# Kernel tuning notes

Measured on AMD Instinct MI355X. Metric: run time of the kernel, lower is better.

Reference implementation:

```python
import jax, jax.numpy as jnp
import numpy as np

NUM_USER = 10000
NUM_ITEM = 30000
N = NUM_USER + NUM_ITEM          # total nodes
DIM = 64                          # dim_E == dim_C
E = 500000                        # user-item interactions
NUM_ROUTING = 3
ALPHA_THR = 0.5
NEG_SLOPE_ATTN = 0.2              # GAT attention leaky slope
NEG_SLOPE_ACT = 0.01              # F.leaky_relu_ default


def l2norm(x, eps=1e-12):
    n = jnp.linalg.norm(x, axis=-1, keepdims=True)
    return x / jnp.maximum(n, eps)


def seg_softmax(score, seg):
    # numerically-stable softmax over edges grouped by destination node
    m = jax.ops.segment_max(score, seg, num_segments=N)
    e = jnp.exp(score - m[seg])
    s = jax.ops.segment_sum(e, seg, num_segments=N)
    return e / (s[seg] + 1e-16)


def gat_ori(x, W, src, dst):
    # GATConv_ori: dot-product attention, softmax per destination, scatter-add
    h = x @ W                                     # [N, C]
    score = jax.nn.leaky_relu(jnp.sum(h[dst] * h[src], -1), NEG_SLOPE_ATTN)
    alpha = seg_softmax(score, dst)               # [2E]
    return jax.ops.segment_sum(alpha[:, None] * h[src], dst, num_segments=N)


def gat_pre(x, y, z, W, src, dst):
    # GATConv_pre: primary-modality attention modulated by cross-modal gate (reattn)
    hx = x @ W
    sx = jnp.sum(hx[dst] * hx[src], -1)
    sy = jnp.sum(y[dst] * y[src], -1)
    sz = jnp.sum(z[dst] * z[src], -1)
    alpha = seg_softmax(jax.nn.leaky_relu(sx, NEG_SLOPE_ATTN), dst)
    gate = jax.nn.sigmoid(0.5 * (sy + sz))
    alpha = jnp.where(gate > ALPHA_THR, alpha * gate, alpha)
    return jax.ops.segment_sum(alpha[:, None] * hx[src], dst, num_segments=N)


def cgcn(pref, feat, pref2, feat2, pref3, feat3, src, dst, Wpre, Wori):
    x = jnp.concatenate([pref, feat], 0)
    y = jnp.concatenate([pref2, feat2], 0)
    z = jnp.concatenate([pref3, feat3], 0)
    x = l2norm(gat_pre(x, y, z, Wpre, src, dst))
    for _ in range(NUM_ROUTING):
        x = l2norm(x + gat_ori(x, Wori, src, dst))
    return x


def gcn_conv(x, W, src, dst):
    return jax.ops.segment_sum((x @ W)[src], dst, num_segments=N)


def real_gcn(id_emb, Wg, src, dst):
    x = l2norm(id_emb)
    h1 = jax.nn.leaky_relu(gcn_conv(x, Wg[0], src, dst), NEG_SLOPE_ACT)
    h2 = jax.nn.leaky_relu(gcn_conv(h1, Wg[1], src, dst), NEG_SLOPE_ACT)
    h3 = gcn_conv(h1, Wg[2], src, dst)
    return x + h1 + h2 + h3


def setup_inputs() -> dict:
    key = jax.random.key(0)
    ks = jax.random.split(key, 16)
    users = jax.random.randint(ks[0], (E,), 0, NUM_USER)
    items = jax.random.randint(ks[1], (E,), NUM_USER, N)
    edge_index = jnp.stack([users, items]).astype(jnp.int64)
    s = 0.05
    return {
        'edge_index': edge_index,
        'v_feat': jax.random.normal(ks[2], (NUM_ITEM, 128), jnp.float32),
        'a_feat': jax.random.normal(ks[3], (NUM_ITEM, 128), jnp.float32),
        't_feat': jax.random.normal(ks[4], (NUM_ITEM, 100), jnp.float32),
        'pref_v': jax.random.normal(ks[5], (NUM_USER, DIM), jnp.float32) * s,
        'pref_a': jax.random.normal(ks[6], (NUM_USER, DIM), jnp.float32) * s,
        'pref_t': jax.random.normal(ks[7], (NUM_USER, DIM), jnp.float32) * s,
        'mlp_v_w': jax.random.normal(ks[8], (DIM, 128), jnp.float32) * s,
        'mlp_v_b': jnp.zeros((DIM,), jnp.float32),
        'mlp_a_w': jax.random.normal(ks[9], (DIM, 128), jnp.float32) * s,
        'mlp_a_b': jnp.zeros((DIM,), jnp.float32),
        'mlp_t_w': jax.random.normal(ks[10], (DIM, 100), jnp.float32) * s,
        'mlp_t_b': jnp.zeros((DIM,), jnp.float32),
        'pre_w': jax.random.normal(ks[11], (3, DIM, DIM), jnp.float32) * s,
        'ori_w': jax.random.normal(ks[12], (3, DIM, DIM), jnp.float32) * s,
        'gcn_w': jax.random.normal(ks[13], (3, DIM, DIM), jnp.float32) * s,
        'id_embedding': jax.random.normal(ks[14], (N, DIM), jnp.float32) * s,
    }


def reference(edge_index, v_feat, a_feat, t_feat, pref_v, pref_a, pref_t,
              mlp_v_w, mlp_v_b, mlp_a_w, mlp_a_b, mlp_t_w, mlp_t_b,
              pre_w, ori_w, gcn_w, id_embedding):
    # symmetrize edges (cat with flipped); no self-loops possible (bipartite)
    src = jnp.concatenate([edge_index[0], edge_index[1]])
    dst = jnp.concatenate([edge_index[1], edge_index[0]])

    fv = l2norm(jax.nn.leaky_relu(v_feat @ mlp_v_w.T + mlp_v_b, NEG_SLOPE_ACT))
    fa = l2norm(jax.nn.leaky_relu(a_feat @ mlp_a_w.T + mlp_a_b, NEG_SLOPE_ACT))
    ft = l2norm(jax.nn.leaky_relu(t_feat @ mlp_t_w.T + mlp_t_b, NEG_SLOPE_ACT))
    pv, pa, pt = l2norm(pref_v), l2norm(pref_a), l2norm(pref_t)

    v_rep = cgcn(pv, fv, pa, fa, pt, ft, src, dst, pre_w[0], ori_w[0])
    a_rep = cgcn(pa, fa, pv, fv, pt, ft, src, dst, pre_w[1], ori_w[1])
    t_rep = cgcn(pt, ft, pa, fa, pv, fv, src, dst, pre_w[2], ori_w[2])
    id_rep = real_gcn(id_embedding, gcn_w, src, dst)

    return jnp.concatenate([id_rep, v_rep, a_rep, t_rep], axis=1)  # [N, 4*DIM]
```

## Files before the change

kernel.cpp:

```cpp
#include <hip/hip_runtime.h>
#include <hip/hip_fp16.h>
#include <math.h>

#define NUSER 10000
#define NITEM 30000
#define NN    40000
#define DD    64
#define PLANE ((size_t)NN * DD)

typedef _Float16 hv2 __attribute__((ext_vector_type(2)));
union U2H { unsigned u; hv2 v; __half2 hh; };

#if defined(__has_builtin)
#if __has_builtin(__builtin_amdgcn_fdot2)
#define HAS_FDOT2 1
#endif
#endif

__device__ __forceinline__ float fdot2u(unsigned a, unsigned b, float c) {
#ifdef HAS_FDOT2
    U2H x, y;
    x.u = a;
    y.u = b;
    return __builtin_amdgcn_fdot2(x.v, y.v, c, false);
#else
    U2H x, y;
    x.u = a;
    y.u = b;
    float2 fa = __half22float2(x.hh), fb = __half22float2(y.hh);
    return c + fa.x * fb.x + fa.y * fb.y;
#endif
}

__device__ __forceinline__ float dot8(uint4 a, uint4 b) {
    float d = fdot2u(a.x, b.x, 0.f);
    d = fdot2u(a.y, b.y, d);
    d = fdot2u(a.z, b.z, d);
    d = fdot2u(a.w, b.w, d);
    return d;
}

__device__ __forceinline__ __half2 uh(unsigned u) { U2H x; x.u = u; return x.hh; }
__device__ __forceinline__ unsigned hu(__half2 h) { U2H x; x.hh = h; return x.u; }
__device__ __forceinline__ __half2 h2rx(__half2 v, int m) {
    return __hadd2(v, uh((unsigned)__shfl_xor((int)hu(v), m, 64)));
}

__device__ __forceinline__ float wsum(float v) {
#pragma unroll
    for (int o = 32; o > 0; o >>= 1) v += __shfl_xor(v, o, 64);
    return v;
}
__device__ __forceinline__ float qsum8(float v) {
    v += __shfl_xor(v, 1, 64);
    v += __shfl_xor(v, 2, 64);
    v += __shfl_xor(v, 4, 64);
    return v;
}
__device__ __forceinline__ float gsum8(float v) {
    v += __shfl_xor(v, 8, 64);
    v += __shfl_xor(v, 16, 64);
    v += __shfl_xor(v, 32, 64);
    return v;
}

__device__ __forceinline__ int nodeperm(int i) {
    return ((i & 3) == 0) ? (i >> 2) : (NUSER + i - 1 - (i >> 2));
}

__global__ void k_hist(const int* ei, int E2, int E, int* cnt) {
    int i = blockIdx.x * blockDim.x + threadIdx.x;
    if (i >= E2) return;
    int d = (i < E) ? ei[E + i] : ei[i - E];
    atomicAdd(&cnt[d], 1);
}

__global__ void k_bsum(const int* __restrict__ cnt, int* __restrict__ bsum, int n, int chunk) {
    __shared__ int wsh[4];
    int b = blockIdx.x, tid = threadIdx.x;
    int base = b * chunk, end = min(n, base + chunk);
    int s = 0;
    for (int i = base + tid; i < end; i += 256) s += cnt[i];
#pragma unroll
    for (int o = 32; o > 0; o >>= 1) s += __shfl_xor(s, o, 64);
    if ((tid & 63) == 0) wsh[tid >> 6] = s;
    __syncthreads();
    if (tid == 0) bsum[b] = wsh[0] + wsh[1] + wsh[2] + wsh[3];
}

__global__ void k_bscan(int* bsum, int nb, int* rp_end) {
    int lane = threadIdx.x;
    int v = (lane < nb) ? bsum[lane] : 0;
    int orig = v;
#pragma unroll
    for (int o = 1; o < 64; o <<= 1) {
        int y = __shfl_up(v, o, 64);
        if (lane >= o) v += y;
    }
    if (lane < nb) bsum[lane] = v - orig;
    if (lane == 63) *rp_end = v;
}

__global__ void k_apply(const int* __restrict__ cnt, const int* __restrict__ boff,
                        int* __restrict__ rp, int n, int chunk) {
    __shared__ int buf[256];
    __shared__ int csh;
    int b = blockIdx.x, tid = threadIdx.x;
    int base = b * chunk, end = min(n, base + chunk);
    int carry = boff[b];
    for (int t0 = base; t0 < end; t0 += 256) {
        int i = t0 + tid;
        int v = (i < end) ? cnt[i] : 0;
        int x = v;
        buf[tid] = x;
        __syncthreads();
        for (int o = 1; o < 256; o <<= 1) {
            int y = (tid >= o) ? buf[tid - o] : 0;
            __syncthreads();
            x += y;
            buf[tid] = x;
            __syncthreads();
        }
        if (i < end) rp[i] = carry + x - v;
        __syncthreads();
        if (tid == 255) csh = carry + x;
        __syncthreads();
        carry = csh;
    }
}

__global__ void k_scatter(const int* ei, int E2, int E, const int* rp, int* fill, int* col) {
    int i = blockIdx.x * blockDim.x + threadIdx.x;
    if (i >= E2) return;
    int j = (i < E) ? i : i - E;
    int s = (i < E) ? ei[j] : ei[E + j];
    int d = (i < E) ? ei[E + j] : ei[j];
    int pos = rp[d] + atomicAdd(&fill[d], 1);
    col[pos] = s;
}

__global__ void k_prep_pref(const float* __restrict__ pv, const float* __restrict__ pa,
                            const float* __restrict__ pt, __half* __restrict__ M) {
    int t = blockIdx.x * blockDim.x + threadIdx.x;
    int w = t >> 6, lane = t & 63, nw = (gridDim.x * blockDim.x) >> 6;
    for (int r = w; r < NUSER; r += nw) {
        float a = pv[(size_t)r * DD + lane];
        float b = pa[(size_t)r * DD + lane];
        float c = pt[(size_t)r * DD + lane];
        float sa = a * a, sb = b * b, sc = c * c;
#pragma unroll
        for (int o = 32; o > 0; o >>= 1) {
            sa += __shfl_xor(sa, o, 64);
            sb += __shfl_xor(sb, o, 64);
            sc += __shfl_xor(sc, o, 64);
        }
        size_t base = (size_t)r * 3 * DD + lane;
        M[base] = __float2half(a / fmaxf(sqrtf(sa), 1e-12f));
        M[base + DD] = __float2half(b / fmaxf(sqrtf(sb), 1e-12f));
        M[base + 2 * DD] = __float2half(c / fmaxf(sqrtf(sc), 1e-12f));
    }
}

template <int K>
__global__ void k_mlp(const float* __restrict__ feat, const float* __restrict__ W,
                      const float* __restrict__ bias, __half* __restrict__ M, int mo) {
    constexpr int K4 = K / 4;
    __shared__ float4 Wl[K4][DD];
    __shared__ float4 rbuf[4][2][K4];
    int t = threadIdx.x, wib = t >> 6, lane = t & 63;
    for (int i = t; i < DD * K4; i += 256) {
        int c = i / K4, k4 = i - c * K4;
        Wl[k4][c] = *(const float4*)(W + (size_t)c * K + k4 * 4);
    }
    __syncthreads();
    float b = bias[lane];
    const int stride = gridDim.x * 4;
    int r = blockIdx.x * 4 + wib;
    float4 v = {0.f, 0.f, 0.f, 0.f};
    if (r < NITEM && lane < K4) v = *(const float4*)(feat + (size_t)r * K + lane * 4);
    int cur = 0;
    for (; r < NITEM; r += stride) {
        if (lane < K4) rbuf[wib][cur][lane] = v;
        int rn = r + stride;
        if (rn < NITEM && lane < K4) v = *(const float4*)(feat + (size_t)rn * K + lane * 4);
        asm volatile("s_waitcnt lgkmcnt(0)" ::: "memory");
        float acc = b;
#pragma unroll
        for (int k4 = 0; k4 < K4; k4++) {
            float4 x4 = rbuf[wib][cur][k4];
            float4 w4 = Wl[k4][lane];
            acc += x4.x * w4.x + x4.y * w4.y + x4.z * w4.z + x4.w * w4.w;
        }
        float h = acc > 0.f ? acc : 0.01f * acc;
        float n = sqrtf(wsum(h * h));
        M[((size_t)(NUSER + r) * 3 + mo) * DD + lane] = __float2half(h / fmaxf(n, 1e-12f));
        cur ^= 1;
    }
}

__global__ void k_gemm_h3(const __half* __restrict__ x3, const float* __restrict__ W3,
                          __half* __restrict__ o3) {
    __shared__ float rowbuf[4][DD];
    int mo = blockIdx.y;
    const float* W = W3 + (size_t)mo * 4096;
    int t = threadIdx.x, wib = t >> 6, lane = t & 63;
    float Wc[DD];
#pragma unroll
    for (int k = 0; k < DD; k++) Wc[k] = W[k * DD + lane];
    for (int r = blockIdx.x * 4 + wib; r < NN; r += gridDim.x * 4) {
        size_t idx = ((size_t)r * 3 + mo) * DD + lane;
        rowbuf[wib][lane] = __half2float(x3[idx]);
        asm volatile("s_waitcnt lgkmcnt(0)" ::: "memory");
        float acc = 0.f;
#pragma unroll
        for (int k4 = 0; k4 < DD / 4; k4++) {
            float4 xq = *(const float4*)&rowbuf[wib][k4 * 4];
            acc += xq.x * Wc[k4 * 4] + xq.y * Wc[k4 * 4 + 1] + xq.z * Wc[k4 * 4 + 2] +
                   xq.w * Wc[k4 * 4 + 3];
        }
        o3[idx] = __float2half(acc);
    }
}

__global__ void k_gemm_f2(const float* __restrict__ x, const float* __restrict__ W2,
                          __half* __restrict__ o2) {
    __shared__ float rowbuf[4][DD];
    int mo = blockIdx.y;
    const float* W = W2 + (size_t)mo * 4096;
    int t = threadIdx.x, wib = t >> 6, lane = t & 63;
    float Wc[DD];
#pragma unroll
    for (int k = 0; k < DD; k++) Wc[k] = W[k * DD + lane];
    for (int r = blockIdx.x * 4 + wib; r < NN; r += gridDim.x * 4) {
        rowbuf[wib][lane] = x[(size_t)r * DD + lane];
        asm volatile("s_waitcnt lgkmcnt(0)" ::: "memory");
        float acc = 0.f;
#pragma unroll
        for (int k4 = 0; k4 < DD / 4; k4++) {
            float4 xq = *(const float4*)&rowbuf[wib][k4 * 4];
            acc += xq.x * Wc[k4 * 4] + xq.y * Wc[k4 * 4 + 1] + xq.z * Wc[k4 * 4 + 2] +
                   xq.w * Wc[k4 * 4 + 3];
        }
        o2[((size_t)r * 2 + mo) * DD + lane] = __float2half(acc);
    }
}

__global__ void k_gemm_id(const float* __restrict__ x, const float* __restrict__ W,
                          __half* __restrict__ hout, float* __restrict__ xnorm) {
    __shared__ float rowbuf[4][DD];
    int t = threadIdx.x, wib = t >> 6, lane = t & 63;
    float Wc[DD];
#pragma unroll
    for (int k = 0; k < DD; k++) Wc[k] = W[k * DD + lane];
    for (int r = blockIdx.x * 4 + wib; r < NN; r += gridDim.x * 4) {
        float xv = x[(size_t)r * DD + lane];
        float n = sqrtf(wsum(xv * xv));
        xv /= fmaxf(n, 1e-12f);
        xnorm[(size_t)r * DD + lane] = xv;
        rowbuf[wib][lane] = xv;
        asm volatile("s_waitcnt lgkmcnt(0)" ::: "memory");
        float acc = 0.f;
#pragma unroll
        for (int k4 = 0; k4 < DD / 4; k4++) {
            float4 xq = *(const float4*)&rowbuf[wib][k4 * 4];
            acc += xq.x * Wc[k4 * 4] + xq.y * Wc[k4 * 4 + 1] + xq.z * Wc[k4 * 4 + 2] +
                   xq.w * Wc[k4 * 4 + 3];
        }
        hout[(size_t)r * DD + lane] = __float2half(acc);
    }
}

__device__ __forceinline__ float gatef(float ssum) {
    float gate = 1.f / (1.f + __expf(-0.5f * ssum));
    return gate > 0.5f ? gate : 1.f;
}

__global__ void k_edgedot3(const __half* __restrict__ M, const int* __restrict__ rp,
                           const int* __restrict__ col, __half* __restrict__ gf4) {
    int t = blockIdx.x * blockDim.x + threadIdx.x;
    int wv = t >> 6, lane = t & 63, nw = (gridDim.x * blockDim.x) >> 6;
    int g = lane >> 3, q = lane & 7;
    for (int w0 = wv; w0 < NN; w0 += nw) {
        int n = nodeperm(w0);
        int e0 = rp[n], e1 = rp[n + 1];
        if (e0 == e1) continue;
        const uint4* trow = (const uint4*)(M + (size_t)n * 192);
        uint4 tv = trow[q], ta = trow[q + 8], tt = trow[q + 16];
        for (int eb = e0 + g; eb < e1; eb += 8) {
            int sn = col[eb];
            const uint4* srow = (const uint4*)(M + (size_t)sn * 192);
            uint4 sv = srow[q], sa = srow[q + 8], st = srow[q + 16];
            float dv = dot8(tv, sv), da = dot8(ta, sa), dt = dot8(tt, st);
            dv = qsum8(dv);
            da = qsum8(da);
            dt = qsum8(dt);
            if (q == 0) {
                U2H p01, p2;
                p01.hh = __floats2half2_rn(gatef(da + dt), gatef(dv + dt));
                p2.hh = __floats2half2_rn(gatef(da + dv), 0.f);
                *(uint2*)(gf4 + (size_t)eb * 4) = make_uint2(p01.u, p2.u);
            }
        }
    }
}

__global__ void k_gat_pre3(const __half* __restrict__ h3, const __half* __restrict__ gf4,
                           const int* __restrict__ rp, const int* __restrict__ col,
                           __half* __restrict__ x3h) {
    int t = blockIdx.x * blockDim.x + threadIdx.x;
    int wv = t >> 6, lane = t & 63, nw = (gridDim.x * blockDim.x) >> 6;
    int g = lane >> 3, q = lane & 7;
    const __half2 z = __floats2half2_rn(0.f, 0.f);
    for (int w0 = wv; w0 < NN; w0 += nw) {
        int n = nodeperm(w0);
        int e0 = rp[n], e1 = rp[n + 1];
        const uint4* hrow = (const uint4*)(h3 + (size_t)n * 192);
        uint4 hd0 = hrow[q], hd1 = hrow[q + 8], hd2 = hrow[q + 16];
        float s0 = 0.f, s1 = 0.f, s2 = 0.f;
        __half2 a0[4] = {z, z, z, z}, a1[4] = {z, z, z, z}, a2[4] = {z, z, z, z};
        for (int eb = e0 + g; eb < e1; eb += 8) {
            int sn = col[eb];
            const uint4* srow = (const uint4*)(h3 + (size_t)sn * 192);
            uint4 v0 = srow[q], v1 = srow[q + 8], v2 = srow[q + 16];
            uint2 gv = *(const uint2*)(gf4 + (size_t)eb * 4);
            float d0 = dot8(hd0, v0), d1 = dot8(hd1, v1), d2 = dot8(hd2, v2);
            d0 = qsum8(d0);
            d1 = qsum8(d1);
            d2 = qsum8(d2);
            float2 g01 = __half22float2(uh(gv.x));
            float g2 = __half22float2(uh(gv.y)).x;
            float sc0 = d0 > 0.f ? d0 : 0.2f * d0;
            float sc1 = d1 > 0.f ? d1 : 0.2f * d1;
            float sc2 = d2 > 0.f ? d2 : 0.2f * d2;
            float p0 = __expf(sc0), p1 = __expf(sc1), p2 = __expf(sc2);
            s0 += p0;
            s1 += p1;
            s2 += p2;
            __half2 ph0 = __float2half2_rn(p0 * g01.x);
            __half2 ph1 = __float2half2_rn(p1 * g01.y);
            __half2 ph2 = __float2half2_rn(p2 * g2);
            a0[0] = __hfma2(ph0, uh(v0.x), a0[0]);
            a0[1] = __hfma2(ph0, uh(v0.y), a0[1]);
            a0[2] = __hfma2(ph0, uh(v0.z), a0[2]);
            a0[3] = __hfma2(ph0, uh(v0.w), a0[3]);
            a1[0] = __hfma2(ph1, uh(v1.x), a1[0]);
            a1[1] = __hfma2(ph1, uh(v1.y), a1[1]);
            a1[2] = __hfma2(ph1, uh(v1.z), a1[2]);
            a1[3] = __hfma2(ph1, uh(v1.w), a1[3]);
            a2[0] = __hfma2(ph2, uh(v2.x), a2[0]);
            a2[1] = __hfma2(ph2, uh(v2.y), a2[1]);
            a2[2] = __hfma2(ph2, uh(v2.z), a2[2]);
            a2[3] = __hfma2(ph2, uh(v2.w), a2[3]);
        }
        s0 = gsum8(s0);
        s1 = gsum8(s1);
        s2 = gsum8(s2);
#pragma unroll
        for (int j = 0; j < 4; j++) {
            a0[j] = h2rx(h2rx(h2rx(a0[j], 8), 16), 32);
            a1[j] = h2rx(h2rx(h2rx(a1[j], 8), 16), 32);
            a2[j] = h2rx(h2rx(h2rx(a2[j], 8), 16), 32);
        }
        float i0 = 1.f / (s0 + 1e-16f), i1 = 1.f / (s1 + 1e-16f), i2 = 1.f / (s2 + 1e-16f);
        float o0[8], o1[8], o2[8];
#pragma unroll
        for (int j = 0; j < 4; j++) {
            float2 f0 = __half22float2(a0[j]);
            float2 f1 = __half22float2(a1[j]);
            float2 f2 = __half22float2(a2[j]);
            o0[2 * j] = f0.x * i0;
            o0[2 * j + 1] = f0.y * i0;
            o1[2 * j] = f1.x * i1;
            o1[2 * j + 1] = f1.y * i1;
            o2[2 * j] = f2.x * i2;
            o2[2 * j + 1] = f2.y * i2;
        }
        float n0 = 0.f, n1 = 0.f, n2 = 0.f;
#pragma unroll
        for (int k = 0; k < 8; k++) {
            n0 += o0[k] * o0[k];
            n1 += o1[k] * o1[k];
            n2 += o2[k] * o2[k];
        }
        n0 = qsum8(n0);
        n1 = qsum8(n1);
        n2 = qsum8(n2);
        float r0 = 1.f / fmaxf(sqrtf(n0), 1e-12f);
        float r1 = 1.f / fmaxf(sqrtf(n1), 1e-12f);
        float r2 = 1.f / fmaxf(sqrtf(n2), 1e-12f);
        if (g == 0) {
            uint4* orow = (uint4*)(x3h + (size_t)n * 192);
            uint4 w0_, w1_, w2_;
            w0_.x = hu(__floats2half2_rn(o0[0] * r0, o0[1] * r0));
            w0_.y = hu(__floats2half2_rn(o0[2] * r0, o0[3] * r0));
            w0_.z = hu(__floats2half2_rn(o0[4] * r0, o0[5] * r0));
            w0_.w = hu(__floats2half2_rn(o0[6] * r0, o0[7] * r0));
            w1_.x = hu(__floats2half2_rn(o1[0] * r1, o1[1] * r1));
            w1_.y = hu(__floats2half2_rn(o1[2] * r1, o1[3] * r1));
            w1_.z = hu(__floats2half2_rn(o1[4] * r1, o1[5] * r1));
            w1_.w = hu(__floats2half2_rn(o1[6] * r1, o1[7] * r1));
            w2_.x = hu(__floats2half2_rn(o2[0] * r2, o2[1] * r2));
            w2_.y = hu(__floats2half2_rn(o2[2] * r2, o2[3] * r2));
            w2_.z = hu(__floats2half2_rn(o2[4] * r2, o2[5] * r2));
            w2_.w = hu(__floats2half2_rn(o2[6] * r2, o2[7] * r2));
            orow[q] = w0_;
            orow[q + 8] = w1_;
            orow[q + 16] = w2_;
        }
    }
}

__global__ void k_gat_ori3(const __half* __restrict__ h3, const __half* __restrict__ x3h,
                           const int* __restrict__ rp, const int* __restrict__ col,
                           __half* __restrict__ xout, float* __restrict__ fout) {
    int t = blockIdx.x * blockDim.x + threadIdx.x;
    int wv = t >> 6, lane = t & 63, nw = (gridDim.x * blockDim.x) >> 6;
    int g = lane >> 3, q = lane & 7;
    const __half2 z = __floats2half2_rn(0.f, 0.f);
    for (int w0 = wv; w0 < NN; w0 += nw) {
        int n = nodeperm(w0);
        int e0 = rp[n], e1 = rp[n + 1];
        const uint4* hrow = (const uint4*)(h3 + (size_t)n * 192);
        uint4 hd0 = hrow[q], hd1 = hrow[q + 8], hd2 = hrow[q + 16];
        float s0 = 0.f, s1 = 0.f, s2 = 0.f;
        __half2 a0[4] = {z, z, z, z}, a1[4] = {z, z, z, z}, a2[4] = {z, z, z, z};
        for (int eb = e0 + g; eb < e1; eb += 8) {
            int sn = col[eb];
            const uint4* srow = (const uint4*)(h3 + (size_t)sn * 192);
            uint4 v0 = srow[q], v1 = srow[q + 8], v2 = srow[q + 16];
            float d0 = dot8(hd0, v0), d1 = dot8(hd1, v1), d2 = dot8(hd2, v2);
            d0 = qsum8(d0);
            d1 = qsum8(d1);
            d2 = qsum8(d2);
            float sc0 = d0 > 0.f ? d0 : 0.2f * d0;
            float sc1 = d1 > 0.f ? d1 : 0.2f * d1;
            float sc2 = d2 > 0.f ? d2 : 0.2f * d2;
            float p0 = __expf(sc0), p1 = __expf(sc1), p2 = __expf(sc2);
            s0 += p0;
            s1 += p1;
            s2 += p2;
            __half2 ph0 = __float2half2_rn(p0);
            __half2 ph1 = __float2half2_rn(p1);
            __half2 ph2 = __float2half2_rn(p2);
            a0[0] = __hfma2(ph0, uh(v0.x), a0[0]);
            a0[1] = __hfma2(ph0, uh(v0.y), a0[1]);
            a0[2] = __hfma2(ph0, uh(v0.z), a0[2]);
            a0[3] = __hfma2(ph0, uh(v0.w), a0[3]);
            a1[0] = __hfma2(ph1, uh(v1.x), a1[0]);
            a1[1] = __hfma2(ph1, uh(v1.y), a1[1]);
            a1[2] = __hfma2(ph1, uh(v1.z), a1[2]);
            a1[3] = __hfma2(ph1, uh(v1.w), a1[3]);
            a2[0] = __hfma2(ph2, uh(v2.x), a2[0]);
            a2[1] = __hfma2(ph2, uh(v2.y), a2[1]);
            a2[2] = __hfma2(ph2, uh(v2.z), a2[2]);
            a2[3] = __hfma2(ph2, uh(v2.w), a2[3]);
        }
        s0 = gsum8(s0);
        s1 = gsum8(s1);
        s2 = gsum8(s2);
#pragma unroll
        for (int j = 0; j < 4; j++) {
            a0[j] = h2rx(h2rx(h2rx(a0[j], 8), 16), 32);
            a1[j] = h2rx(h2rx(h2rx(a1[j], 8), 16), 32);
            a2[j] = h2rx(h2rx(h2rx(a2[j], 8), 16), 32);
        }
        float i0 = 1.f / (s0 + 1e-16f), i1 = 1.f / (s1 + 1e-16f), i2 = 1.f / (s2 + 1e-16f);
        const uint4* xrow = (const uint4*)(x3h + (size_t)n * 192);
        uint4 xr0 = xrow[q], xr1 = xrow[q + 8], xr2 = xrow[q + 16];
        float o0[8], o1[8], o2[8];
#pragma unroll
        for (int j = 0; j < 4; j++) {
            float2 f0 = __half22float2(a0[j]);
            float2 f1 = __half22float2(a1[j]);
            float2 f2 = __half22float2(a2[j]);
            float2 xf0 = __half22float2(uh(j == 0 ? xr0.x : j == 1 ? xr0.y : j == 2 ? xr0.z : xr0.w));
            float2 xf1 = __half22float2(uh(j == 0 ? xr1.x : j == 1 ? xr1.y : j == 2 ? xr1.z : xr1.w));
            float2 xf2 = __half22float2(uh(j == 0 ? xr2.x : j == 1 ? xr2.y : j == 2 ? xr2.z : xr2.w));
            o0[2 * j] = xf0.x + f0.x * i0;
            o0[2 * j + 1] = xf0.y + f0.y * i0;
            o1[2 * j] = xf1.x + f1.x * i1;
            o1[2 * j + 1] = xf1.y + f1.y * i1;
            o2[2 * j] = xf2.x + f2.x * i2;
            o2[2 * j + 1] = xf2.y + f2.y * i2;
        }
        float n0 = 0.f, n1 = 0.f, n2 = 0.f;
#pragma unroll
        for (int k = 0; k < 8; k++) {
            n0 += o0[k] * o0[k];
            n1 += o1[k] * o1[k];
            n2 += o2[k] * o2[k];
        }
        n0 = qsum8(n0);
        n1 = qsum8(n1);
        n2 = qsum8(n2);
        float r0 = 1.f / fmaxf(sqrtf(n0), 1e-12f);
        float r1 = 1.f / fmaxf(sqrtf(n1), 1e-12f);
        float r2 = 1.f / fmaxf(sqrtf(n2), 1e-12f);
        if (g == 0) {
            if (fout) {
                float* ob = fout + (size_t)n * 256 + 64 + q * 8;
                float4 wa, wb;
                wa = make_float4(o0[0] * r0, o0[1] * r0, o0[2] * r0, o0[3] * r0);
                wb = make_float4(o0[4] * r0, o0[5] * r0, o0[6] * r0, o0[7] * r0);
                *(float4*)(ob) = wa;
                *(float4*)(ob + 4) = wb;
                wa = make_float4(o1[0] * r1, o1[1] * r1, o1[2] * r1, o1[3] * r1);
                wb = make_float4(o1[4] * r1, o1[5] * r1, o1[6] * r1, o1[7] * r1);
                *(float4*)(ob + 64) = wa;
                *(float4*)(ob + 68) = wb;
                wa = make_float4(o2[0] * r2, o2[1] * r2, o2[2] * r2, o2[3] * r2);
                wb = make_float4(o2[4] * r2, o2[5] * r2, o2[6] * r2, o2[7] * r2);
                *(float4*)(ob + 128) = wa;
                *(float4*)(ob + 132) = wb;
            } else {
                uint4* orow = (uint4*)(xout + (size_t)n * 192);
                uint4 w0_, w1_, w2_;
                w0_.x = hu(__floats2half2_rn(o0[0] * r0, o0[1] * r0));
                w0_.y = hu(__floats2half2_rn(o0[2] * r0, o0[3] * r0));
                w0_.z = hu(__floats2half2_rn(o0[4] * r0, o0[5] * r0));
                w0_.w = hu(__floats2half2_rn(o0[6] * r0, o0[7] * r0));
                w1_.x = hu(__floats2half2_rn(o1[0] * r1, o1[1] * r1));
                w1_.y = hu(__floats2half2_rn(o1[2] * r1, o1[3] * r1));
                w1_.z = hu(__floats2half2_rn(o1[4] * r1, o1[5] * r1));
                w1_.w = hu(__floats2half2_rn(o1[6] * r1, o1[7] * r1));
                w2_.x = hu(__floats2half2_rn(o2[0] * r2, o2[1] * r2));
                w2_.y = hu(__floats2half2_rn(o2[2] * r2, o2[3] * r2));
                w2_.z = hu(__floats2half2_rn(o2[4] * r2, o2[5] * r2));
                w2_.w = hu(__floats2half2_rn(o2[6] * r2, o2[7] * r2));
                orow[q] = w0_;
                orow[q + 8] = w1_;
                orow[q + 16] = w2_;
            }
        }
    }
}

__global__ void k_gcn1(const __half* __restrict__ h, const int* __restrict__ rp,
                       const int* __restrict__ col, float* __restrict__ out) {
    int t = blockIdx.x * blockDim.x + threadIdx.x;
    int wv = t >> 6, lane = t & 63, nw = (gridDim.x * blockDim.x) >> 6;
    int g = lane >> 3, q = lane & 7;
    const __half2 z = __floats2half2_rn(0.f, 0.f);
    for (int w0 = wv; w0 < NN; w0 += nw) {
        int n = nodeperm(w0);
        int e0 = rp[n], e1 = rp[n + 1];
        __half2 a[4] = {z, z, z, z};
        for (int eb = e0 + g; eb < e1; eb += 8) {
            int sn = col[eb];
            uint4 v = ((const uint4*)(h + (size_t)sn * DD))[q];
            a[0] = __hadd2(a[0], uh(v.x));
            a[1] = __hadd2(a[1], uh(v.y));
            a[2] = __hadd2(a[2], uh(v.z));
            a[3] = __hadd2(a[3], uh(v.w));
        }
#pragma unroll
        for (int j = 0; j < 4; j++) a[j] = h2rx(h2rx(h2rx(a[j], 8), 16), 32);
        if (g == 0) {
            float o[8];
#pragma unroll
            for (int j = 0; j < 4; j++) {
                float2 f = __half22float2(a[j]);
                o[2 * j] = f.x > 0.f ? f.x : 0.01f * f.x;
                o[2 * j + 1] = f.y > 0.f ? f.y : 0.01f * f.y;
            }
            float* ob = out + (size_t)n * DD + q * 8;
            *(float4*)(ob) = make_float4(o[0], o[1], o[2], o[3]);
            *(float4*)(ob + 4) = make_float4(o[4], o[5], o[6], o[7]);
        }
    }
}

__global__ void k_gcn_final2(const __half* __restrict__ gp, const int* __restrict__ rp,
                             const int* __restrict__ col, const float* __restrict__ x0,
                             const float* __restrict__ h1, float* __restrict__ out) {
    int t = blockIdx.x * blockDim.x + threadIdx.x;
    int wv = t >> 6, lane = t & 63, nw = (gridDim.x * blockDim.x) >> 6;
    int g = lane >> 3, q = lane & 7;
    const __half2 z = __floats2half2_rn(0.f, 0.f);
    for (int w0 = wv; w0 < NN; w0 += nw) {
        int n = nodeperm(w0);
        int e0 = rp[n], e1 = rp[n + 1];
        __half2 aA[4] = {z, z, z, z}, aB[4] = {z, z, z, z};
        for (int eb = e0 + g; eb < e1; eb += 8) {
            int sn = col[eb];
            const uint4* base = (const uint4*)(gp + (size_t)sn * 128);
            uint4 vA = base[q], vB = base[q + 8];
            aA[0] = __hadd2(aA[0], uh(vA.x));
            aA[1] = __hadd2(aA[1], uh(vA.y));
            aA[2] = __hadd2(aA[2], uh(vA.z));
            aA[3] = __hadd2(aA[3], uh(vA.w));
            aB[0] = __hadd2(aB[0], uh(vB.x));
            aB[1] = __hadd2(aB[1], uh(vB.y));
            aB[2] = __hadd2(aB[2], uh(vB.z));
            aB[3] = __hadd2(aB[3], uh(vB.w));
        }
#pragma unroll
        for (int j = 0; j < 4; j++) {
            aA[j] = h2rx(h2rx(h2rx(aA[j], 8), 16), 32);
            aB[j] = h2rx(h2rx(h2rx(aB[j], 8), 16), 32);
        }
        if (g == 0) {
            const float* p0 = x0 + (size_t)n * DD + q * 8;
            const float* p1 = h1 + (size_t)n * DD + q * 8;
            float4 v0a = *(const float4*)(p0), v0b = *(const float4*)(p0 + 4);
            float4 v1a = *(const float4*)(p1), v1b = *(const float4*)(p1 + 4);
            float o[8];
#pragma unroll
            for (int j = 0; j < 4; j++) {
                float2 fA = __half22float2(aA[j]);
                float2 fB = __half22float2(aB[j]);
                float h2x = fA.x > 0.f ? fA.x : 0.01f * fA.x;
                float h2y = fA.y > 0.f ? fA.y : 0.01f * fA.y;
                o[2 * j] = h2x + fB.x;
                o[2 * j + 1] = h2y + fB.y;
            }
            float* ob = out + (size_t)n * 256 + q * 8;
            *(float4*)(ob) = make_float4(o[0] + v0a.x + v1a.x, o[1] + v0a.y + v1a.y,
                                         o[2] + v0a.z + v1a.z, o[3] + v0a.w + v1a.w);
            *(float4*)(ob + 4) = make_float4(o[4] + v0b.x + v1b.x, o[5] + v0b.y + v1b.y,
                                             o[6] + v0b.z + v1b.z, o[7] + v0b.w + v1b.w);
        }
    }
}

extern "C" void kernel_launch(void* const* d_in, const int* in_sizes, int n_in,
                              void* d_out, int out_size, void* d_ws, size_t ws_size,
                              hipStream_t stream) {
    const int* ei       = (const int*)d_in[0];
    const float* v_feat = (const float*)d_in[1];
    const float* a_feat = (const float*)d_in[2];
    const float* t_feat = (const float*)d_in[3];
    const float* pref_v = (const float*)d_in[4];
    const float* pref_a = (const float*)d_in[5];
    const float* pref_t = (const float*)d_in[6];
    const float* mlp_v_w = (const float*)d_in[7];
    const float* mlp_v_b = (const float*)d_in[8];
    const float* mlp_a_w = (const float*)d_in[9];
    const float* mlp_a_b = (const float*)d_in[10];
    const float* mlp_t_w = (const float*)d_in[11];
    const float* mlp_t_b = (const float*)d_in[12];
    const float* pre_w  = (const float*)d_in[13];
    const float* ori_w  = (const float*)d_in[14];
    const float* gcn_w  = (const float*)d_in[15];
    const float* id_emb = (const float*)d_in[16];
    float* out = (float*)d_out;

    const int E2 = in_sizes[0];
    const int E  = E2 / 2;

    char* w = (char*)d_ws;
    auto alloc = [&](size_t bytes) -> void* {
        void* p = (void*)w;
        w += (bytes + 255) & ~(size_t)255;
        return p;
    };
    int* cnt  = (int*)alloc((size_t)NN * 4);
    int* rp   = (int*)alloc((size_t)(NN + 1) * 4);
    int* bsum = (int*)alloc(256);
    int* col  = (int*)alloc((size_t)E2 * 4);
    __half* Mh3  = (__half*)alloc(3 * PLANE * 2);
    __half* hb3h = (__half*)alloc(3 * PLANE * 2);
    __half* x3h  = (__half*)alloc(3 * PLANE * 2);
    __half* gf4  = (__half*)alloc((size_t)E2 * 4 * 2);
    float* x0f = (float*)alloc(PLANE * 4);
    float* h1f = (float*)alloc(PLANE * 4);

    __half* g1 = hb3h;
    __half* gpair = hb3h + PLANE;

    const int NBLK = 64, CHUNK = (NN + NBLK - 1) / NBLK;
    hipMemsetAsync(cnt, 0, (size_t)NN * 4, stream);
    k_hist<<<(E2 + 255) / 256, 256, 0, stream>>>(ei, E2, E, cnt);
    k_bsum<<<NBLK, 256, 0, stream>>>(cnt, bsum, NN, CHUNK);
    k_bscan<<<1, 64, 0, stream>>>(bsum, NBLK, rp + NN);
    k_apply<<<NBLK, 256, 0, stream>>>(cnt, bsum, rp, NN, CHUNK);
    hipMemsetAsync(cnt, 0, (size_t)NN * 4, stream);
    k_scatter<<<(E2 + 255) / 256, 256, 0, stream>>>(ei, E2, E, rp, cnt, col);

    k_prep_pref<<<640, 256, 0, stream>>>(pref_v, pref_a, pref_t, Mh3);
    k_mlp<128><<<1024, 256, 0, stream>>>(v_feat, mlp_v_w, mlp_v_b, Mh3, 0);
    k_mlp<128><<<1024, 256, 0, stream>>>(a_feat, mlp_a_w, mlp_a_b, Mh3, 1);
    k_mlp<100><<<1024, 256, 0, stream>>>(t_feat, mlp_t_w, mlp_t_b, Mh3, 2);

    const int GB = (NN + 3) / 4;

    k_edgedot3<<<GB, 256, 0, stream>>>(Mh3, rp, col, gf4);

    dim3 g3(1280, 3);
    k_gemm_h3<<<g3, 256, 0, stream>>>(Mh3, pre_w, hb3h);
    k_gat_pre3<<<GB, 256, 0, stream>>>(hb3h, gf4, rp, col, x3h);
    for (int it = 0; it < 3; it++) {
        k_gemm_h3<<<g3, 256, 0, stream>>>(x3h, ori_w, hb3h);
        if (it < 2)
            k_gat_ori3<<<GB, 256, 0, stream>>>(hb3h, x3h, rp, col, x3h, nullptr);
        else
            k_gat_ori3<<<GB, 256, 0, stream>>>(hb3h, x3h, rp, col, nullptr, out);
    }

    k_gemm_id<<<1280, 256, 0, stream>>>(id_emb, gcn_w, g1, x0f);
    k_gcn1<<<GB, 256, 0, stream>>>(g1, rp, col, h1f);
    dim3 g2(1280, 2);
    k_gemm_f2<<<g2, 256, 0, stream>>>(h1f, gcn_w + 4096, gpair);
    k_gcn_final2<<<GB, 256, 0, stream>>>(gpair, rp, col, x0f, h1f, out);
}
```

Baseline: 661.5 us.

## Use MFMA for per-modality GEMMs and reuse histogram slots in CSR scatter

Replaces the scalar per-row 64x64 GEMM (weights held in registers, row staged through LDS) with a wavefront-level MFMA 16x16x32 fp16 kernel that processes 16-row tiles and keeps the weight fragments in registers. Separately, the histogram kernel now records each edge's atomic slot so the scatter kernel can place edges without a second memset and second round of atomics. The MFMA path rounds weights to fp16, which adds precision loss, and its output stores are scattered 2-byte writes. The slot buffer adds an extra E2-sized int array in workspace.

```diff
diff --git a/kernel.cpp b/kernel.cpp
--- a/kernel.cpp
+++ b/kernel.cpp
@@ -9,6 +9,8 @@
 #define PLANE ((size_t)NN * DD)
 
 typedef _Float16 hv2 __attribute__((ext_vector_type(2)));
+typedef _Float16 half8v __attribute__((ext_vector_type(8)));
+typedef float float4v __attribute__((ext_vector_type(4)));
 union U2H { unsigned u; hv2 v; __half2 hh; };
 
 #if defined(__has_builtin)
@@ -68,11 +70,11 @@
     return ((i & 3) == 0) ? (i >> 2) : (NUSER + i - 1 - (i >> 2));
 }
 
-__global__ void k_hist(const int* ei, int E2, int E, int* cnt) {
+__global__ void k_hist(const int* ei, int E2, int E, int* cnt, int* posw) {
     int i = blockIdx.x * blockDim.x + threadIdx.x;
     if (i >= E2) return;
     int d = (i < E) ? ei[E + i] : ei[i - E];
-    atomicAdd(&cnt[d], 1);
+    posw[i] = atomicAdd(&cnt[d], 1);
 }
 
 __global__ void k_bsum(const int* __restrict__ cnt, int* __restrict__ bsum, int n, int chunk) {
@@ -129,14 +131,14 @@
     }
 }
 
-__global__ void k_scatter(const int* ei, int E2, int E, const int* rp, int* fill, int* col) {
+__global__ void k_scatter(const int* ei, int E2, int E, const int* rp,
+                          const int* __restrict__ posw, int* col) {
     int i = blockIdx.x * blockDim.x + threadIdx.x;
     if (i >= E2) return;
     int j = (i < E) ? i : i - E;
     int s = (i < E) ? ei[j] : ei[E + j];
     int d = (i < E) ? ei[E + j] : ei[j];
-    int pos = rp[d] + atomicAdd(&fill[d], 1);
-    col[pos] = s;
+    col[rp[d] + posw[i]] = s;
 }
 
 __global__ void k_prep_pref(const float* __restrict__ pv, const float* __restrict__ pa,
@@ -198,27 +200,42 @@
     }
 }
 
-__global__ void k_gemm_h3(const __half* __restrict__ x3, const float* __restrict__ W3,
-                          __half* __restrict__ o3) {
-    __shared__ float rowbuf[4][DD];
+__global__ void k_gemm_mfma(const __half* __restrict__ x3, const float* __restrict__ W3,
+                            __half* __restrict__ o3) {
     int mo = blockIdx.y;
     const float* W = W3 + (size_t)mo * 4096;
-    int t = threadIdx.x, wib = t >> 6, lane = t & 63;
-    float Wc[DD];
-#pragma unroll
-    for (int k = 0; k < DD; k++) Wc[k] = W[k * DD + lane];
-    for (int r = blockIdx.x * 4 + wib; r < NN; r += gridDim.x * 4) {
-        size_t idx = ((size_t)r * 3 + mo) * DD + lane;
-        rowbuf[wib][lane] = __half2float(x3[idx]);
-        asm volatile("s_waitcnt lgkmcnt(0)" ::: "memory");
-        float acc = 0.f;
-#pragma unroll
-        for (int k4 = 0; k4 < DD / 4; k4++) {
-            float4 xq = *(const float4*)&rowbuf[wib][k4 * 4];
-            acc += xq.x * Wc[k4 * 4] + xq.y * Wc[k4 * 4 + 1] + xq.z * Wc[k4 * 4 + 2] +
-                   xq.w * Wc[k4 * 4 + 3];
-        }
-        o3[idx] = __float2half(acc);
+    int t = threadIdx.x, wv = t >> 6, lane = t & 63;
+    int lr = lane & 15, lg = lane >> 4;
+    half8v b[4][2];
+#pragma unroll
+    for (int ct = 0; ct < 4; ct++)
+#pragma unroll
+        for (int kh = 0; kh < 2; kh++)
+#pragma unroll
+            for (int i = 0; i < 8; i++)
+                b[ct][kh][i] = (_Float16)W[(kh * 32 + lg * 8 + i) * 64 + ct * 16 + lr];
+    const int NT = NN / 16;
+    for (int rt = blockIdx.x * 4 + wv; rt < NT; rt += gridDim.x * 4) {
+        const __half* xr = x3 + ((size_t)(rt * 16 + lr) * 3 + mo) * DD + lg * 8;
+        half8v a0 = *(const half8v*)xr;
+        half8v a1 = *(const half8v*)(xr + 32);
+        float4v acc0 = {0.f, 0.f, 0.f, 0.f}, acc1 = acc0, acc2 = acc0, acc3 = acc0;
+        acc0 = __builtin_amdgcn_mfma_f32_16x16x32_f16(a0, b[0][0], acc0, 0, 0, 0);
+        acc1 = __builtin_amdgcn_mfma_f32_16x16x32_f16(a0, b[1][0], acc1, 0, 0, 0);
+        acc2 = __builtin_amdgcn_mfma_f32_16x16x32_f16(a0, b[2][0], acc2, 0, 0, 0);
+        acc3 = __builtin_amdgcn_mfma_f32_16x16x32_f16(a0, b[3][0], acc3, 0, 0, 0);
+        acc0 = __builtin_amdgcn_mfma_f32_16x16x32_f16(a1, b[0][1], acc0, 0, 0, 0);
+        acc1 = __builtin_amdgcn_mfma_f32_16x16x32_f16(a1, b[1][1], acc1, 0, 0, 0);
+        acc2 = __builtin_amdgcn_mfma_f32_16x16x32_f16(a1, b[2][1], acc2, 0, 0, 0);
+        acc3 = __builtin_amdgcn_mfma_f32_16x16x32_f16(a1, b[3][1], acc3, 0, 0, 0);
+#pragma unroll
+        for (int i = 0; i < 4; i++) {
+            size_t rbase = ((size_t)(rt * 16 + lg * 4 + i) * 3 + mo) * DD + lr;
+            o3[rbase] = __float2half(acc0[i]);
+            o3[rbase + 16] = __float2half(acc1[i]);
+            o3[rbase + 32] = __float2half(acc2[i]);
+            o3[rbase + 48] = __float2half(acc3[i]);
+        }
     }
 }
 
@@ -658,6 +675,7 @@
     int* rp   = (int*)alloc((size_t)(NN + 1) * 4);
     int* bsum = (int*)alloc(256);
     int* col  = (int*)alloc((size_t)E2 * 4);
+    int* posw = (int*)alloc((size_t)E2 * 4);
     __half* Mh3  = (__half*)alloc(3 * PLANE * 2);
     __half* hb3h = (__half*)alloc(3 * PLANE * 2);
     __half* x3h  = (__half*)alloc(3 * PLANE * 2);
@@ -670,12 +688,11 @@
 
     const int NBLK = 64, CHUNK = (NN + NBLK - 1) / NBLK;
     hipMemsetAsync(cnt, 0, (size_t)NN * 4, stream);
-    k_hist<<<(E2 + 255) / 256, 256, 0, stream>>>(ei, E2, E, cnt);
+    k_hist<<<(E2 + 255) / 256, 256, 0, stream>>>(ei, E2, E, cnt, posw);
     k_bsum<<<NBLK, 256, 0, stream>>>(cnt, bsum, NN, CHUNK);
     k_bscan<<<1, 64, 0, stream>>>(bsum, NBLK, rp + NN);
     k_apply<<<NBLK, 256, 0, stream>>>(cnt, bsum, rp, NN, CHUNK);
-    hipMemsetAsync(cnt, 0, (size_t)NN * 4, stream);
-    k_scatter<<<(E2 + 255) / 256, 256, 0, stream>>>(ei, E2, E, rp, cnt, col);
+    k_scatter<<<(E2 + 255) / 256, 256, 0, stream>>>(ei, E2, E, rp, posw, col);
 
     k_prep_pref<<<640, 256, 0, stream>>>(pref_v, pref_a, pref_t, Mh3);
     k_mlp<128><<<1024, 256, 0, stream>>>(v_feat, mlp_v_w, mlp_v_b, Mh3, 0);
@@ -686,11 +703,11 @@
 
     k_edgedot3<<<GB, 256, 0, stream>>>(Mh3, rp, col, gf4);
 
-    dim3 g3(1280, 3);
-    k_gemm_h3<<<g3, 256, 0, stream>>>(Mh3, pre_w, hb3h);
+    dim3 gm(640, 3);
+    k_gemm_mfma<<<gm, 256, 0, stream>>>(Mh3, pre_w, hb3h);
     k_gat_pre3<<<GB, 256, 0, stream>>>(hb3h, gf4, rp, col, x3h);
     for (int it = 0; it < 3; it++) {
-        k_gemm_h3<<<g3, 256, 0, stream>>>(x3h, ori_w, hb3h);
+        k_gemm_mfma<<<gm, 256, 0, stream>>>(x3h, ori_w, hb3h);
         if (it < 2)
             k_gat_ori3<<<GB, 256, 0, stream>>>(hb3h, x3h, rp, col, x3h, nullptr);
         else
```

Measured after the change: 554.2 us. -16.2%, faster.
